# Performance work log

Measured on AMD Instinct MI355X. Metric: run time of the kernel, lower is better.

## Reference

```python
import jax, jax.numpy as jnp
import numpy as np

B, S, HID = 16, 512, 2048
H = 4
D = HID // H  # 512; module requires S == D
SCALE = 1.0 / np.sqrt(D).astype(np.float32)


def setup_inputs() -> dict:
    key = jax.random.key(0)
    ks = jax.random.split(key, 6)
    std = 0.02
    inp = {"hidden_states": jax.random.normal(ks[0], (B, S, HID), jnp.float32)}
    names = ["q", "k", "v", "ck", "cv"]
    for i, n in enumerate(names):
        inp[f"W{n}"] = jax.random.normal(ks[i + 1], (HID, HID), jnp.float32) * std
        inp[f"b{n}"] = jnp.zeros((HID,), jnp.float32)
    return inp


def _heads(x):
    # [B,S,HID] -> [B,H,S,D]
    return x.reshape(B, S, H, D).transpose(0, 2, 1, 3)


def reference(hidden_states, Wq, bq, Wk, bk, Wv, bv, Wck, bck, Wcv, bcv):
    q = _heads(hidden_states @ Wq.T + bq)
    k = _heads(hidden_states @ Wk.T + bk)
    v = _heads(hidden_states @ Wv.T + bv)
    ck = _heads(hidden_states @ Wck.T + bck)
    cv = _heads(hidden_states @ Wcv.T + bcv)

    # scores1[b,h,q,j] = sum_d Q[b,h,q,d] K[b,h,j,d]
    s1 = jnp.einsum('bhqd,bhjd->bhqj', q, k)
    # scores2 = scores1 @ cube_key^T (valid since S == D)
    s2 = jnp.einsum('bhqj,bhmj->bhqm', s1, ck) * SCALE
    probs = jax.nn.softmax(s2, axis=-1)
    # ctx1 = probs @ V : [B,H,S,D]
    ctx = jnp.einsum('bhqm,bhmd->bhqd', probs, v)
    # ctx2 = ctx1 @ cube_value : [S,D]@[S,D] valid since S == D
    ctx = jnp.einsum('bhqm,bhme->bhqe', ctx, cv)
    # merge heads: [B,H,S,D] -> [B,S,HID]
    return ctx.transpose(0, 2, 1, 3).reshape(B, S, HID)
```

## Files before the change

kernel.cpp:

```cpp
#include <hip/hip_runtime.h>
#include <math.h>


typedef _Float16 f16;
typedef f16 f16x8 __attribute__((ext_vector_type(8)));
typedef float f32x4 __attribute__((ext_vector_type(4)));
typedef float f32x16 __attribute__((ext_vector_type(16)));

#define SB_STRIDE 520
#define BP_HALF   16384
#define CHAIN_LDS ((64 * SB_STRIDE + 2 * BP_HALF) * 2)
#define PROJ_LDS  131072

static constexpr float SCALE = 0.04419417382415922f;

__device__ __forceinline__ void gl_lds16(const f16* g, f16* l)
{
    __builtin_amdgcn_global_load_lds(
        (const __attribute__((address_space(1))) void*)g,
        (__attribute__((address_space(3))) void*)l, 16, 0, 0);
}

__global__ __launch_bounds__(256) void conv_f32_f16(const float* __restrict__ src,
                                                    f16* __restrict__ dst, int n)
{
    int i = (blockIdx.x * 256 + threadIdx.x) * 8;
    if (i + 8 <= n) {
        float4 a = *(const float4*)(src + i);
        float4 b = *(const float4*)(src + i + 4);
        f16 o[8] = {(f16)a.x, (f16)a.y, (f16)a.z, (f16)a.w,
                    (f16)b.x, (f16)b.y, (f16)b.z, (f16)b.w};
        *(int4*)(dst + i) = *(int4*)o;
    }
}

struct ProjPtrs {
    const f16* W[5];
    const float* bias[5];
    f16* dst[5];
};

__global__ __launch_bounds__(512, 2) void proj_f16(const f16* __restrict__ A, ProjPtrs P)
{
    extern __shared__ f16 sm[];
    const int z = blockIdx.z;
    const f16* __restrict__ W = P.W[z];
    const float* __restrict__ bias = P.bias[z];
    f16* __restrict__ dst = P.dst[z];
    const bool tr = (z == 2) || (z == 4);

    const int t    = threadIdx.x;
    const int lane = t & 63;
    const int wave = t >> 6;
    const int wr   = wave >> 2, wc = wave & 3;
    const int bm = blockIdx.y * 256, bn = blockIdx.x * 256;

    const int r16 = lane & 15;
    const int kg  = (lane >> 4) & 3;
    const f16* aB0 = A + (size_t)(bm + wave * 16 + r16) * 2048 + kg * 8;
    const f16* aB1 = aB0 + (size_t)128 * 2048;
    const f16* bB0 = W + (size_t)(bn + wave * 16 + r16) * 2048 + kg * 8;
    const f16* bB1 = bB0 + (size_t)128 * 2048;

#define STAGE(j, k0)                                          \
    {                                                         \
        f16* bp = sm + (j) * 16384 + wave * 512;              \
        gl_lds16(aB0 + (k0), bp);                             \
        gl_lds16(aB1 + (k0), bp + 4096);                      \
        gl_lds16(bB0 + (k0), bp + 8192);                      \
        gl_lds16(bB1 + (k0), bp + 12288);                     \
    }

    f32x4 acc[8][4];
#pragma unroll
    for (int mf = 0; mf < 8; ++mf)
#pragma unroll
        for (int nf = 0; nf < 4; ++nf)
#pragma unroll
            for (int r = 0; r < 4; ++r) acc[mf][nf][r] = 0.f;

    STAGE(0, 0);
    STAGE(1, 32);
    STAGE(2, 64);

    const int lkoff = (lane >> 4) * 128 + r16 * 8;

    for (int kt = 0; kt < 64; ++kt) {
        if (kt < 62)       asm volatile("s_waitcnt vmcnt(8)" ::: "memory");
        else if (kt == 62) asm volatile("s_waitcnt vmcnt(4)" ::: "memory");
        else               asm volatile("s_waitcnt vmcnt(0)" ::: "memory");
        __builtin_amdgcn_s_barrier();
        asm volatile("" ::: "memory");

        if (kt + 3 < 64) STAGE((kt + 3) & 3, (kt + 3) * 32);

        const f16* bufA = sm + (kt & 3) * 16384;
        const f16* bufB = bufA + 8192;

        f16x8 af[8], bf[4];
#pragma unroll
        for (int mf = 0; mf < 8; ++mf)
            af[mf] = *(const f16x8*)(bufA + (wr * 8 + mf) * 512 + lkoff);
#pragma unroll
        for (int nf = 0; nf < 4; ++nf)
            bf[nf] = *(const f16x8*)(bufB + (wc * 4 + nf) * 512 + lkoff);

        __builtin_amdgcn_s_setprio(1);
#pragma unroll
        for (int mf = 0; mf < 8; ++mf)
#pragma unroll
            for (int nf = 0; nf < 4; ++nf)
                acc[mf][nf] = __builtin_amdgcn_mfma_f32_16x16x32_f16(
                    af[mf], bf[nf], acc[mf][nf], 0, 0, 0);
        __builtin_amdgcn_s_setprio(0);
    }
#undef STAGE

    const int wm = wr * 128, wn = wc * 64;
#pragma unroll
    for (int nf = 0; nf < 4; ++nf) {
        int n = bn + wn + nf * 16 + r16;
        float bb = bias[n];
        int h = n >> 9, d = n & 511;
#pragma unroll
        for (int mf = 0; mf < 8; ++mf) {
            int mbase = bm + wm + mf * 16 + (lane >> 4) * 4;
            int b = mbase >> 9, s0 = mbase & 511;
            if (!tr) {
#pragma unroll
                for (int r = 0; r < 4; ++r)
                    dst[(((size_t)(b * 4 + h)) * 512 + s0 + r) * 512 + d] =
                        (f16)(acc[mf][nf][r] + bb);
            } else {
                f16 pk[4];
#pragma unroll
                for (int r = 0; r < 4; ++r) pk[r] = (f16)(acc[mf][nf][r] + bb);
                *(float2*)(dst + (((size_t)(b * 4 + h)) * 512 + d) * 512 + s0) =
                    *(float2*)pk;
            }
        }
    }
}

__device__ __forceinline__ void stage_nt(
    const f16* __restrict__ Bsrc,
    f16* __restrict__ Sb, f16* __restrict__ Bp, int t, f32x16 acc[2][2])
{
    const int lane = t & 63;
    const int wave = t >> 6;
    const int l31  = lane & 31;
    const int l5   = (lane >> 5) * 8;

#pragma unroll
    for (int mt = 0; mt < 2; ++mt)
#pragma unroll
        for (int nt = 0; nt < 2; ++nt)
#pragma unroll
            for (int r = 0; r < 16; ++r) acc[mt][nt][r] = 0.f;

#pragma unroll
    for (int it = 0; it < 4; ++it) {
        int nb = wave * 2 + (it & 1), ks = it >> 1;
        gl_lds16(Bsrc + (size_t)(nb * 32 + l31) * 512 + ks * 16 + l5,
                 Bp + nb * 1024 + ks * 512);
    }

    for (int p = 0; p < 16; ++p) {
        const int k0 = p * 32;
        __syncthreads();
        if (p < 15) {
            f16* nbuf = Bp + ((p + 1) & 1) * BP_HALF;
#pragma unroll
            for (int it = 0; it < 4; ++it) {
                int nb = wave * 2 + (it & 1), ks = it >> 1;
                gl_lds16(Bsrc + (size_t)(nb * 32 + l31) * 512 + k0 + 32 + ks * 16 + l5,
                         nbuf + nb * 1024 + ks * 512);
            }
        }
        const f16* cbuf = Bp + (p & 1) * BP_HALF;
#pragma unroll
        for (int dk = 0; dk < 32; dk += 16) {
            f16x8 af[2], bf[2];
#pragma unroll
            for (int mt = 0; mt < 2; ++mt)
                af[mt] = *(const f16x8*)(Sb + (size_t)(mt * 32 + l31) * SB_STRIDE + k0 + dk + l5);
#pragma unroll
            for (int nt = 0; nt < 2; ++nt)
                bf[nt] = *(const f16x8*)(cbuf + (wave * 2 + nt) * 1024 + (dk >> 4) * 512 + lane * 8);
#pragma unroll
            for (int mt = 0; mt < 2; ++mt)
#pragma unroll
                for (int nt = 0; nt < 2; ++nt)
                    acc[mt][nt] = __builtin_amdgcn_mfma_f32_32x32x16_f16(af[mt], bf[nt], acc[mt][nt], 0, 0, 0);
        }
    }
    __syncthreads();
}

__device__ __forceinline__ void emit_to_S(f16* __restrict__ Sb, const f32x16 acc[2][2],
                                          int t, float scale)
{
    const int lane = t & 63;
    const int wn = (t >> 6) * 64;
#pragma unroll
    for (int mt = 0; mt < 2; ++mt)
#pragma unroll
        for (int nt = 0; nt < 2; ++nt) {
            int col = wn + nt * 32 + (lane & 31);
#pragma unroll
            for (int r = 0; r < 16; ++r) {
                int row = mt * 32 + (r & 3) + 8 * (r >> 2) + 4 * (lane >> 5);
                Sb[(size_t)row * SB_STRIDE + col] = (f16)(acc[mt][nt][r] * scale);
            }
        }
}

__global__ __launch_bounds__(512) void chain_f16(
    const f16* __restrict__ q16, const f16* __restrict__ k16,
    const f16* __restrict__ ck16, const f16* __restrict__ vt16,
    const f16* __restrict__ cvt16, float* __restrict__ out)
{
    extern __shared__ f16 smem[];
    f16* Sb = smem;
    f16* Bp = smem + 64 * SB_STRIDE;
    const int t = threadIdx.x;
    const int bh = blockIdx.x >> 3;
    const int q0 = (blockIdx.x & 7) * 64;
    const size_t SB = 512 * 512;

    const f16* Q = q16 + bh * SB;
    for (int i = t; i < 4096; i += 512) {
        int row = i >> 6, c = (i & 63) * 8;
        *(int4*)(Sb + (size_t)row * SB_STRIDE + c) =
            *(const int4*)(Q + (size_t)(q0 + row) * 512 + c);
    }

    f32x16 acc[2][2];

    stage_nt(k16 + bh * SB, Sb, Bp, t, acc);
    emit_to_S(Sb, acc, t, 1.0f);

    stage_nt(ck16 + bh * SB, Sb, Bp, t, acc);
    emit_to_S(Sb, acc, t, SCALE);
    __syncthreads();

    {
        const int lane = t & 63;
        const int wave = t >> 6;
        for (int rr = 0; rr < 8; ++rr) {
            int r = wave * 8 + rr;
            f16x8 xv = *(const f16x8*)(Sb + (size_t)r * SB_STRIDE + lane * 8);
            float x[8];
            float mx = -1e30f;
#pragma unroll
            for (int j = 0; j < 8; ++j) { x[j] = (float)xv[j]; mx = fmaxf(mx, x[j]); }
#pragma unroll
            for (int o = 32; o > 0; o >>= 1) mx = fmaxf(mx, __shfl_xor(mx, o));
            float s = 0.f;
#pragma unroll
            for (int j = 0; j < 8; ++j) { x[j] = __expf(x[j] - mx); s += x[j]; }
#pragma unroll
            for (int o = 32; o > 0; o >>= 1) s += __shfl_xor(s, o);
            float inv = 1.0f / s;
            f16x8 ov;
#pragma unroll
            for (int j = 0; j < 8; ++j) ov[j] = (f16)(x[j] * inv);
            *(f16x8*)(Sb + (size_t)r * SB_STRIDE + lane * 8) = ov;
        }
    }

    stage_nt(vt16 + bh * SB, Sb, Bp, t, acc);
    emit_to_S(Sb, acc, t, 1.0f);

    stage_nt(cvt16 + bh * SB, Sb, Bp, t, acc);
    {
        const int lane = t & 63;
        const int wn = (t >> 6) * 64;
        int b = bh >> 2, h = bh & 3;
#pragma unroll
        for (int mt = 0; mt < 2; ++mt)
#pragma unroll
            for (int nt = 0; nt < 2; ++nt) {
                int col = h * 512 + wn + nt * 32 + (lane & 31);
#pragma unroll
                for (int r = 0; r < 16; ++r) {
                    int row = q0 + mt * 32 + (r & 3) + 8 * (r >> 2) + 4 * (lane >> 5);
                    out[((size_t)b * 512 + row) * 2048 + col] = acc[mt][nt][r];
                }
            }
    }
}

extern "C" void kernel_launch(void* const* d_in, const int* in_sizes, int n_in,
                              void* d_out, int out_size, void* d_ws, size_t ws_size,
                              hipStream_t stream)
{
    const float* hs = (const float*)d_in[0];
    const float* Wf[5] = {(const float*)d_in[1], (const float*)d_in[3],
                          (const float*)d_in[5], (const float*)d_in[7],
                          (const float*)d_in[9]};
    const float* bf[5] = {(const float*)d_in[2], (const float*)d_in[4],
                          (const float*)d_in[6], (const float*)d_in[8],
                          (const float*)d_in[10]};
    float* out = (float*)d_out;

    hipFuncSetAttribute((const void*)chain_f16,
                        hipFuncAttributeMaxDynamicSharedMemorySize, CHAIN_LDS);
    hipFuncSetAttribute((const void*)proj_f16,
                        hipFuncAttributeMaxDynamicSharedMemorySize, PROJ_LDS);

    f16* ws = (f16*)d_ws;
    const size_t WELEM = 2048ULL * 2048;
    const size_t FULLACT = 64ULL * 512 * 512;

    f16* W16[5];
    for (int i = 0; i < 5; ++i) W16[i] = ws + i * WELEM;
    f16* after_w = ws + 5 * WELEM;

    for (int i = 0; i < 5; ++i)
        conv_f32_f16<<<dim3(WELEM / 2048), 256, 0, stream>>>(Wf[i], W16[i], (int)WELEM);

    size_t full_need = (5 * WELEM + FULLACT + 5 * FULLACT) * sizeof(f16);
    if (ws_size >= full_need) {
        f16* hs16 = after_w;
        f16* act[5];
        for (int i = 0; i < 5; ++i) act[i] = after_w + FULLACT + i * FULLACT;

        conv_f32_f16<<<dim3(FULLACT / 2048), 256, 0, stream>>>(hs, hs16, (int)FULLACT);

        ProjPtrs P;
        for (int i = 0; i < 5; ++i) { P.W[i] = W16[i]; P.bias[i] = bf[i]; P.dst[i] = act[i]; }
        proj_f16<<<dim3(8, 32, 5), 512, PROJ_LDS, stream>>>(hs16, P);

        chain_f16<<<dim3(512), 512, CHAIN_LDS, stream>>>(
            act[0], act[1], act[3], act[2], act[4], out);
    } else {
        const size_t CHROW = 1048576ULL;
        const size_t CHACT = 4ULL * 512 * 512;
        f16* hs16c = after_w;
        f16* act[5];
        for (int i = 0; i < 5; ++i) act[i] = after_w + CHROW + i * CHACT;

        ProjPtrs P;
        for (int i = 0; i < 5; ++i) { P.W[i] = W16[i]; P.bias[i] = bf[i]; P.dst[i] = act[i]; }

        for (int c = 0; c < 16; ++c) {
            conv_f32_f16<<<dim3(CHROW / 2048), 256, 0, stream>>>(
                hs + c * CHROW, hs16c, (int)CHROW);
            proj_f16<<<dim3(8, 2, 5), 512, PROJ_LDS, stream>>>(hs16c, P);
            chain_f16<<<dim3(32), 512, CHAIN_LDS, stream>>>(
                act[0], act[1], act[3], act[2], act[4], out + c * CHROW);
        }
    }

    (void)in_sizes; (void)n_in; (void)out_size;
}
```

Before: 783.2 us.

## Restructure projection GEMM main loop into 64-wide K steps with quadrant-staged loads

The projection GEMM now handles 64-element K tiles using two double-buffered LDS stages instead of 32-element tiles in a four-deep ring. Each K step is split into four MFMA quadrants, and the global-to-LDS loads for the next tiles are interleaved between them, with barriers and waitcnts separating the phases. The aim is to halve the number of loop iterations and overlap memory traffic with compute at a finer grain. In exchange the loop has more barriers per iteration and holds more fragment registers.

```diff
diff --git a/kernel.cpp b/kernel.cpp
--- a/kernel.cpp
+++ b/kernel.cpp
@@ -54,21 +54,24 @@
     const int wave = t >> 6;
     const int wr   = wave >> 2, wc = wave & 3;
     const int bm = blockIdx.y * 256, bn = blockIdx.x * 256;
-
     const int r16 = lane & 15;
-    const int kg  = (lane >> 4) & 3;
-    const f16* aB0 = A + (size_t)(bm + wave * 16 + r16) * 2048 + kg * 8;
-    const f16* aB1 = aB0 + (size_t)128 * 2048;
-    const f16* bB0 = W + (size_t)(bn + wave * 16 + r16) * 2048 + kg * 8;
-    const f16* bB1 = bB0 + (size_t)128 * 2048;
-
-#define STAGE(j, k0)                                          \
-    {                                                         \
-        f16* bp = sm + (j) * 16384 + wave * 512;              \
-        gl_lds16(aB0 + (k0), bp);                             \
-        gl_lds16(aB1 + (k0), bp + 4096);                      \
-        gl_lds16(bB0 + (k0), bp + 8192);                      \
-        gl_lds16(bB1 + (k0), bp + 12288);                     \
+    const int kq  = lane >> 4;
+
+    const f16* gA = A + (size_t)(bm + (wave >> 1) * 16 + r16) * 2048 + ((wave & 1) * 4 + kq) * 8;
+    const f16* gB = W + (size_t)(bn + (wave >> 1) * 16 + r16) * 2048 + ((wave & 1) * 4 + kq) * 8;
+    const int stoff = wave * 512;
+
+#define STG_A(c, h, tt)                                                     \
+    {                                                                       \
+        f16* d_ = sm + (c) * 32768 + (h) * 8192 + stoff;                    \
+        gl_lds16(gA + (size_t)((h) * 128) * 2048 + (tt) * 64, d_);          \
+        gl_lds16(gA + (size_t)((h) * 128 + 64) * 2048 + (tt) * 64, d_ + 4096); \
+    }
+#define STG_B(c, h, tt)                                                     \
+    {                                                                       \
+        f16* d_ = sm + (c) * 32768 + 16384 + (h) * 8192 + stoff;            \
+        gl_lds16(gB + (size_t)((h) * 128) * 2048 + (tt) * 64, d_);          \
+        gl_lds16(gB + (size_t)((h) * 128 + 64) * 2048 + (tt) * 64, d_ + 4096); \
     }
 
     f32x4 acc[8][4];
@@ -79,42 +82,119 @@
 #pragma unroll
             for (int r = 0; r < 4; ++r) acc[mf][nf][r] = 0.f;
 
-    STAGE(0, 0);
-    STAGE(1, 32);
-    STAGE(2, 64);
-
-    const int lkoff = (lane >> 4) * 128 + r16 * 8;
-
-    for (int kt = 0; kt < 64; ++kt) {
-        if (kt < 62)       asm volatile("s_waitcnt vmcnt(8)" ::: "memory");
-        else if (kt == 62) asm volatile("s_waitcnt vmcnt(4)" ::: "memory");
-        else               asm volatile("s_waitcnt vmcnt(0)" ::: "memory");
-        __builtin_amdgcn_s_barrier();
-        asm volatile("" ::: "memory");
-
-        if (kt + 3 < 64) STAGE((kt + 3) & 3, (kt + 3) * 32);
-
-        const f16* bufA = sm + (kt & 3) * 16384;
-        const f16* bufB = bufA + 8192;
-
-        f16x8 af[8], bf[4];
-#pragma unroll
-        for (int mf = 0; mf < 8; ++mf)
-            af[mf] = *(const f16x8*)(bufA + (wr * 8 + mf) * 512 + lkoff);
-#pragma unroll
-        for (int nf = 0; nf < 4; ++nf)
-            bf[nf] = *(const f16x8*)(bufB + (wc * 4 + nf) * 512 + lkoff);
-
+    STG_A(0, 0, 0); STG_A(0, 1, 0); STG_B(0, 0, 0); STG_B(0, 1, 0);
+    STG_A(1, 0, 1); STG_A(1, 1, 1);
+    asm volatile("s_waitcnt vmcnt(4)" ::: "memory");
+    __builtin_amdgcn_s_barrier();
+    asm volatile("" ::: "memory");
+
+    const int aoff = kq * 128 + r16 * 8;
+
+    f16x8 af[8][2], bf[4][2];
+
+    for (int kt = 0; kt < 32; ++kt) {
+        const int cur = kt & 1, nxt = cur ^ 1;
+        const f16* pa = sm + cur * 32768 + wr * 8192 + aoff;
+        const f16* pb = sm + cur * 32768 + 16384 + (wc >> 1) * 8192 + (wc & 1) * 4096 + aoff;
+
+#pragma unroll
+        for (int mf = 0; mf < 4; ++mf)
+#pragma unroll
+            for (int dk = 0; dk < 2; ++dk)
+                af[mf][dk] = *(const f16x8*)(pa + mf * 1024 + dk * 512);
+#pragma unroll
+        for (int nf = 0; nf < 2; ++nf)
+#pragma unroll
+            for (int dk = 0; dk < 2; ++dk)
+                bf[nf][dk] = *(const f16x8*)(pb + nf * 1024 + dk * 512);
+        if (kt + 1 < 32) STG_B(nxt, 0, kt + 1);
+        asm volatile("" ::: "memory");
+        __builtin_amdgcn_s_barrier();
+        asm volatile("s_waitcnt lgkmcnt(0)" ::: "memory");
+        __builtin_amdgcn_sched_barrier(0);
         __builtin_amdgcn_s_setprio(1);
 #pragma unroll
-        for (int mf = 0; mf < 8; ++mf)
-#pragma unroll
-            for (int nf = 0; nf < 4; ++nf)
-                acc[mf][nf] = __builtin_amdgcn_mfma_f32_16x16x32_f16(
-                    af[mf], bf[nf], acc[mf][nf], 0, 0, 0);
+        for (int mf = 0; mf < 4; ++mf)
+#pragma unroll
+            for (int nf = 0; nf < 2; ++nf)
+#pragma unroll
+                for (int dk = 0; dk < 2; ++dk)
+                    acc[mf][nf] = __builtin_amdgcn_mfma_f32_16x16x32_f16(
+                        af[mf][dk], bf[nf][dk], acc[mf][nf], 0, 0, 0);
         __builtin_amdgcn_s_setprio(0);
-    }
-#undef STAGE
+        asm volatile("" ::: "memory");
+        __builtin_amdgcn_s_barrier();
+        asm volatile("" ::: "memory");
+
+#pragma unroll
+        for (int mf = 4; mf < 8; ++mf)
+#pragma unroll
+            for (int dk = 0; dk < 2; ++dk)
+                af[mf][dk] = *(const f16x8*)(pa + mf * 1024 + dk * 512);
+        if (kt + 1 < 32) STG_B(nxt, 1, kt + 1);
+        asm volatile("" ::: "memory");
+        __builtin_amdgcn_s_barrier();
+        asm volatile("s_waitcnt lgkmcnt(0)" ::: "memory");
+        __builtin_amdgcn_sched_barrier(0);
+        __builtin_amdgcn_s_setprio(1);
+#pragma unroll
+        for (int mf = 4; mf < 8; ++mf)
+#pragma unroll
+            for (int nf = 0; nf < 2; ++nf)
+#pragma unroll
+                for (int dk = 0; dk < 2; ++dk)
+                    acc[mf][nf] = __builtin_amdgcn_mfma_f32_16x16x32_f16(
+                        af[mf][dk], bf[nf][dk], acc[mf][nf], 0, 0, 0);
+        __builtin_amdgcn_s_setprio(0);
+        asm volatile("" ::: "memory");
+        __builtin_amdgcn_s_barrier();
+        asm volatile("" ::: "memory");
+
+#pragma unroll
+        for (int nf = 2; nf < 4; ++nf)
+#pragma unroll
+            for (int dk = 0; dk < 2; ++dk)
+                bf[nf][dk] = *(const f16x8*)(pb + nf * 1024 + dk * 512);
+        if (kt + 2 < 32) STG_A(cur, 0, kt + 2);
+        asm volatile("" ::: "memory");
+        __builtin_amdgcn_s_barrier();
+        asm volatile("s_waitcnt lgkmcnt(0)" ::: "memory");
+        __builtin_amdgcn_sched_barrier(0);
+        __builtin_amdgcn_s_setprio(1);
+#pragma unroll
+        for (int mf = 0; mf < 4; ++mf)
+#pragma unroll
+            for (int nf = 2; nf < 4; ++nf)
+#pragma unroll
+                for (int dk = 0; dk < 2; ++dk)
+                    acc[mf][nf] = __builtin_amdgcn_mfma_f32_16x16x32_f16(
+                        af[mf][dk], bf[nf][dk], acc[mf][nf], 0, 0, 0);
+        __builtin_amdgcn_s_setprio(0);
+        asm volatile("" ::: "memory");
+        __builtin_amdgcn_s_barrier();
+        asm volatile("" ::: "memory");
+
+        if (kt + 2 < 32) STG_A(cur, 1, kt + 2);
+        if (kt < 30) asm volatile("s_waitcnt vmcnt(4)" ::: "memory");
+        else         asm volatile("s_waitcnt vmcnt(0)" ::: "memory");
+        __builtin_amdgcn_s_barrier();
+        asm volatile("" ::: "memory");
+        __builtin_amdgcn_s_setprio(1);
+#pragma unroll
+        for (int mf = 4; mf < 8; ++mf)
+#pragma unroll
+            for (int nf = 2; nf < 4; ++nf)
+#pragma unroll
+                for (int dk = 0; dk < 2; ++dk)
+                    acc[mf][nf] = __builtin_amdgcn_mfma_f32_16x16x32_f16(
+                        af[mf][dk], bf[nf][dk], acc[mf][nf], 0, 0, 0);
+        __builtin_amdgcn_s_setprio(0);
+        asm volatile("" ::: "memory");
+        __builtin_amdgcn_s_barrier();
+        asm volatile("" ::: "memory");
+    }
+#undef STG_A
+#undef STG_B
 
     const int wm = wr * 128, wn = wc * 64;
 #pragma unroll
```

After: 765.0 us. 1.02x faster.

## Shrink projection tiles and load chain B operands directly into registers

Applied to the files above, without the earlier changes.

The projection GEMM tile drops from 256x256 to 128x256 with a 3-stage LDS ring, which cuts LDS use and raises launch bounds to 4 blocks per CU. The grid grows to match. In the chain kernel the B operands are no longer staged through LDS with global_load_lds. Each wave now loads its B fragments straight from global memory into double-buffered registers, which frees the LDS staging buffer and raises occupancy. The cost is lower reuse per tile in the projection, more global traffic and register pressure in the chain, and extra block-wide barriers around the emit steps.

```diff
diff --git a/kernel.cpp b/kernel.cpp
--- a/kernel.cpp
+++ b/kernel.cpp
@@ -8,9 +8,8 @@
 typedef float f32x16 __attribute__((ext_vector_type(16)));
 
 #define SB_STRIDE 520
-#define BP_HALF   16384
-#define CHAIN_LDS ((64 * SB_STRIDE + 2 * BP_HALF) * 2)
-#define PROJ_LDS  131072
+#define CHAIN_LDS (64 * SB_STRIDE * 2)
+#define PROJ_LDS  73728
 
 static constexpr float SCALE = 0.04419417382415922f;
 
@@ -40,7 +39,7 @@
     f16* dst[5];
 };
 
-__global__ __launch_bounds__(512, 2) void proj_f16(const f16* __restrict__ A, ProjPtrs P)
+__global__ __launch_bounds__(512, 4) void proj_f16(const f16* __restrict__ A, ProjPtrs P)
 {
     extern __shared__ f16 sm[];
     const int z = blockIdx.z;
@@ -53,77 +52,78 @@
     const int lane = t & 63;
     const int wave = t >> 6;
     const int wr   = wave >> 2, wc = wave & 3;
-    const int bm = blockIdx.y * 256, bn = blockIdx.x * 256;
-
+    const int bm = blockIdx.y * 128, bn = blockIdx.x * 256;
     const int r16 = lane & 15;
-    const int kg  = (lane >> 4) & 3;
-    const f16* aB0 = A + (size_t)(bm + wave * 16 + r16) * 2048 + kg * 8;
-    const f16* aB1 = aB0 + (size_t)128 * 2048;
-    const f16* bB0 = W + (size_t)(bn + wave * 16 + r16) * 2048 + kg * 8;
-    const f16* bB1 = bB0 + (size_t)128 * 2048;
-
-#define STAGE(j, k0)                                          \
-    {                                                         \
-        f16* bp = sm + (j) * 16384 + wave * 512;              \
-        gl_lds16(aB0 + (k0), bp);                             \
-        gl_lds16(aB1 + (k0), bp + 4096);                      \
-        gl_lds16(bB0 + (k0), bp + 8192);                      \
-        gl_lds16(bB1 + (k0), bp + 12288);                     \
-    }
-
-    f32x4 acc[8][4];
-#pragma unroll
-    for (int mf = 0; mf < 8; ++mf)
+    const int kq  = lane >> 4;
+
+    const f16* gA = A + (size_t)(bm + wave * 16 + r16) * 2048 + kq * 8;
+    const f16* gB = W + (size_t)(bn + wave * 16 + r16) * 2048 + kq * 8;
+
+#define STAGE(b, tt)                                                \
+    {                                                               \
+        f16* d_ = sm + (b) * 12288 + wave * 512;                    \
+        gl_lds16(gA + (tt) * 32, d_);                               \
+        gl_lds16(gB + (tt) * 32, d_ + 4096);                        \
+        gl_lds16(gB + (size_t)128 * 2048 + (tt) * 32, d_ + 8192);   \
+    }
+
+    f32x4 acc[4][4];
+#pragma unroll
+    for (int mf = 0; mf < 4; ++mf)
 #pragma unroll
         for (int nf = 0; nf < 4; ++nf)
 #pragma unroll
             for (int r = 0; r < 4; ++r) acc[mf][nf][r] = 0.f;
 
     STAGE(0, 0);
-    STAGE(1, 32);
-    STAGE(2, 64);
-
-    const int lkoff = (lane >> 4) * 128 + r16 * 8;
-
+    STAGE(1, 1);
+
+    const int lkoff = kq * 128 + r16 * 8;
+
+    int cb = 0;
     for (int kt = 0; kt < 64; ++kt) {
-        if (kt < 62)       asm volatile("s_waitcnt vmcnt(8)" ::: "memory");
-        else if (kt == 62) asm volatile("s_waitcnt vmcnt(4)" ::: "memory");
-        else               asm volatile("s_waitcnt vmcnt(0)" ::: "memory");
+        if (kt < 63) asm volatile("s_waitcnt vmcnt(3)" ::: "memory");
+        else         asm volatile("s_waitcnt vmcnt(0)" ::: "memory");
         __builtin_amdgcn_s_barrier();
         asm volatile("" ::: "memory");
 
-        if (kt + 3 < 64) STAGE((kt + 3) & 3, (kt + 3) * 32);
-
-        const f16* bufA = sm + (kt & 3) * 16384;
-        const f16* bufB = bufA + 8192;
-
-        f16x8 af[8], bf[4];
-#pragma unroll
-        for (int mf = 0; mf < 8; ++mf)
-            af[mf] = *(const f16x8*)(bufA + (wr * 8 + mf) * 512 + lkoff);
+        if (kt + 2 < 64) {
+            int sb = (cb >= 1) ? cb - 1 : 2;
+            STAGE(sb, kt + 2);
+        }
+
+        const f16* bufA = sm + cb * 12288;
+        const f16* bufB = bufA + 4096;
+
+        f16x8 af[4], bf[4];
+#pragma unroll
+        for (int mf = 0; mf < 4; ++mf)
+            af[mf] = *(const f16x8*)(bufA + (wr * 4 + mf) * 512 + lkoff);
 #pragma unroll
         for (int nf = 0; nf < 4; ++nf)
             bf[nf] = *(const f16x8*)(bufB + (wc * 4 + nf) * 512 + lkoff);
 
         __builtin_amdgcn_s_setprio(1);
 #pragma unroll
-        for (int mf = 0; mf < 8; ++mf)
+        for (int mf = 0; mf < 4; ++mf)
 #pragma unroll
             for (int nf = 0; nf < 4; ++nf)
                 acc[mf][nf] = __builtin_amdgcn_mfma_f32_16x16x32_f16(
                     af[mf], bf[nf], acc[mf][nf], 0, 0, 0);
         __builtin_amdgcn_s_setprio(0);
+
+        cb = (cb == 2) ? 0 : cb + 1;
     }
 #undef STAGE
 
-    const int wm = wr * 128, wn = wc * 64;
+    const int wm = wr * 64, wn = wc * 64;
 #pragma unroll
     for (int nf = 0; nf < 4; ++nf) {
         int n = bn + wn + nf * 16 + r16;
         float bb = bias[n];
         int h = n >> 9, d = n & 511;
 #pragma unroll
-        for (int mf = 0; mf < 8; ++mf) {
+        for (int mf = 0; mf < 4; ++mf) {
             int mbase = bm + wm + mf * 16 + (lane >> 4) * 4;
             int b = mbase >> 9, s0 = mbase & 511;
             if (!tr) {
@@ -142,9 +142,9 @@
     }
 }
 
-__device__ __forceinline__ void stage_nt(
-    const f16* __restrict__ Bsrc,
-    f16* __restrict__ Sb, f16* __restrict__ Bp, int t, f32x16 acc[2][2])
+__device__ __forceinline__ void stage_ntr(const f16* __restrict__ Bsrc,
+                                          const f16* __restrict__ Sb,
+                                          int t, f32x16 acc[2][2])
 {
     const int lane = t & 63;
     const int wave = t >> 6;
@@ -158,43 +158,37 @@
 #pragma unroll
             for (int r = 0; r < 16; ++r) acc[mt][nt][r] = 0.f;
 
-#pragma unroll
-    for (int it = 0; it < 4; ++it) {
-        int nb = wave * 2 + (it & 1), ks = it >> 1;
-        gl_lds16(Bsrc + (size_t)(nb * 32 + l31) * 512 + ks * 16 + l5,
-                 Bp + nb * 1024 + ks * 512);
-    }
-
+    const f16* b0 = Bsrc + (size_t)(wave * 64 + l31) * 512 + l5;
+    const f16* b1 = Bsrc + (size_t)(wave * 64 + 32 + l31) * 512 + l5;
+
+    f16x8 bfA[2][2], bfB[2][2];
+
+#define LDP(S, pp)                                              \
+    do {                                                        \
+        S[0][0] = *(const f16x8*)(b0 + (pp) * 32);              \
+        S[0][1] = *(const f16x8*)(b0 + (pp) * 32 + 16);         \
+        S[1][0] = *(const f16x8*)(b1 + (pp) * 32);              \
+        S[1][1] = *(const f16x8*)(b1 + (pp) * 32 + 16);         \
+    } while (0)
+
+    LDP(bfA, 0);
+    LDP(bfB, 1);
+
+#pragma unroll
     for (int p = 0; p < 16; ++p) {
-        const int k0 = p * 32;
-        __syncthreads();
-        if (p < 15) {
-            f16* nbuf = Bp + ((p + 1) & 1) * BP_HALF;
-#pragma unroll
-            for (int it = 0; it < 4; ++it) {
-                int nb = wave * 2 + (it & 1), ks = it >> 1;
-                gl_lds16(Bsrc + (size_t)(nb * 32 + l31) * 512 + k0 + 32 + ks * 16 + l5,
-                         nbuf + nb * 1024 + ks * 512);
-            }
-        }
-        const f16* cbuf = Bp + (p & 1) * BP_HALF;
-#pragma unroll
-        for (int dk = 0; dk < 32; dk += 16) {
-            f16x8 af[2], bf[2];
-#pragma unroll
-            for (int mt = 0; mt < 2; ++mt)
-                af[mt] = *(const f16x8*)(Sb + (size_t)(mt * 32 + l31) * SB_STRIDE + k0 + dk + l5);
-#pragma unroll
-            for (int nt = 0; nt < 2; ++nt)
-                bf[nt] = *(const f16x8*)(cbuf + (wave * 2 + nt) * 1024 + (dk >> 4) * 512 + lane * 8);
-#pragma unroll
-            for (int mt = 0; mt < 2; ++mt)
-#pragma unroll
-                for (int nt = 0; nt < 2; ++nt)
-                    acc[mt][nt] = __builtin_amdgcn_mfma_f32_32x32x16_f16(af[mt], bf[nt], acc[mt][nt], 0, 0, 0);
-        }
-    }
-    __syncthreads();
+        f16x8 (&S)[2][2] = (p & 1) ? bfB : bfA;
+#pragma unroll
+        for (int dkh = 0; dkh < 2; ++dkh) {
+            f16x8 af0 = *(const f16x8*)(Sb + (size_t)l31 * SB_STRIDE + p * 32 + dkh * 16 + l5);
+            f16x8 af1 = *(const f16x8*)(Sb + (size_t)(32 + l31) * SB_STRIDE + p * 32 + dkh * 16 + l5);
+            acc[0][0] = __builtin_amdgcn_mfma_f32_32x32x16_f16(af0, S[0][dkh], acc[0][0], 0, 0, 0);
+            acc[0][1] = __builtin_amdgcn_mfma_f32_32x32x16_f16(af0, S[1][dkh], acc[0][1], 0, 0, 0);
+            acc[1][0] = __builtin_amdgcn_mfma_f32_32x32x16_f16(af1, S[0][dkh], acc[1][0], 0, 0, 0);
+            acc[1][1] = __builtin_amdgcn_mfma_f32_32x32x16_f16(af1, S[1][dkh], acc[1][1], 0, 0, 0);
+        }
+        if (p + 2 < 16) LDP(S, p + 2);
+    }
+#undef LDP
 }
 
 __device__ __forceinline__ void emit_to_S(f16* __restrict__ Sb, const f32x16 acc[2][2],
@@ -215,14 +209,13 @@
         }
 }
 
-__global__ __launch_bounds__(512) void chain_f16(
+__global__ __launch_bounds__(512, 4) void chain_f16(
     const f16* __restrict__ q16, const f16* __restrict__ k16,
     const f16* __restrict__ ck16, const f16* __restrict__ vt16,
     const f16* __restrict__ cvt16, float* __restrict__ out)
 {
     extern __shared__ f16 smem[];
     f16* Sb = smem;
-    f16* Bp = smem + 64 * SB_STRIDE;
     const int t = threadIdx.x;
     const int bh = blockIdx.x >> 3;
     const int q0 = (blockIdx.x & 7) * 64;
@@ -234,13 +227,17 @@
         *(int4*)(Sb + (size_t)row * SB_STRIDE + c) =
             *(const int4*)(Q + (size_t)(q0 + row) * 512 + c);
     }
+    __syncthreads();
 
     f32x16 acc[2][2];
 
-    stage_nt(k16 + bh * SB, Sb, Bp, t, acc);
+    stage_ntr(k16 + bh * SB, Sb, t, acc);
+    __syncthreads();
     emit_to_S(Sb, acc, t, 1.0f);
-
-    stage_nt(ck16 + bh * SB, Sb, Bp, t, acc);
+    __syncthreads();
+
+    stage_ntr(ck16 + bh * SB, Sb, t, acc);
+    __syncthreads();
     emit_to_S(Sb, acc, t, SCALE);
     __syncthreads();
 
@@ -268,11 +265,14 @@
             *(f16x8*)(Sb + (size_t)r * SB_STRIDE + lane * 8) = ov;
         }
     }
-
-    stage_nt(vt16 + bh * SB, Sb, Bp, t, acc);
+    __syncthreads();
+
+    stage_ntr(vt16 + bh * SB, Sb, t, acc);
+    __syncthreads();
     emit_to_S(Sb, acc, t, 1.0f);
-
-    stage_nt(cvt16 + bh * SB, Sb, Bp, t, acc);
+    __syncthreads();
+
+    stage_ntr(cvt16 + bh * SB, Sb, t, acc);
     {
         const int lane = t & 63;
         const int wn = (t >> 6) * 64;
@@ -330,7 +330,7 @@
 
         ProjPtrs P;
         for (int i = 0; i < 5; ++i) { P.W[i] = W16[i]; P.bias[i] = bf[i]; P.dst[i] = act[i]; }
-        proj_f16<<<dim3(8, 32, 5), 512, PROJ_LDS, stream>>>(hs16, P);
+        proj_f16<<<dim3(8, 64, 5), 512, PROJ_LDS, stream>>>(hs16, P);
 
         chain_f16<<<dim3(512), 512, CHAIN_LDS, stream>>>(
             act[0], act[1], act[3], act[2], act[4], out);
@@ -347,7 +347,7 @@
         for (int c = 0; c < 16; ++c) {
             conv_f32_f16<<<dim3(CHROW / 2048), 256, 0, stream>>>(
                 hs + c * CHROW, hs16c, (int)CHROW);
-            proj_f16<<<dim3(8, 2, 5), 512, PROJ_LDS, stream>>>(hs16c, P);
+            proj_f16<<<dim3(8, 16, 5), 512, PROJ_LDS, stream>>>(hs16c, P);
             chain_f16<<<dim3(32), 512, CHAIN_LDS, stream>>>(
                 act[0], act[1], act[3], act[2], act[4], out + c * CHROW);
         }
```

After: 837.2 us. +6.9%, slower.
